# Kernel optimization log

Measured on AMD Instinct MI355X. Metric: run time of the kernel, lower is better.

## Reference

```python
import jax, jax.numpy as jnp
import numpy as np

B, C, H, W = 4, 256, 64, 64


def setup_inputs() -> dict:
    key = jax.random.key(0)
    ks = jax.random.split(key, 6)
    scale = 1.0 / np.sqrt(C)  # keep logits in a sane range
    x = jax.random.normal(ks[0], (B, C, H, W), dtype=jnp.float32)
    wq = jax.random.normal(ks[1], (C, C), dtype=jnp.float32) * scale
    wk = jax.random.normal(ks[2], (C, C), dtype=jnp.float32) * scale
    wv = jax.random.normal(ks[3], (C, C), dtype=jnp.float32) * scale
    wp = jax.random.normal(ks[4], (C, C), dtype=jnp.float32) * scale
    zb = jnp.zeros((C,), dtype=jnp.float32)
    return {"x": x, "wq": wq, "bq": zb, "wk": wk, "bk": zb,
            "wv": wv, "bv": zb, "wp": wp, "bp": zb}


def reference(x, wq, bq, wk, bk, wv, bv, wp, bp):
    b, c, h, w = x.shape
    n = h * w
    xf = x.reshape(b, c, n)  # [b, c, n] spatial tokens
    # 1x1 convs == channel-mixing GEMMs (weight layout: [out_c, in_c])
    q = jnp.einsum('oc,bcn->bon', wq, xf) + bq[:, None]
    k = jnp.einsum('oc,bcn->bon', wk, xf) + bk[:, None]
    v = jnp.einsum('oc,bcn->bon', wv, xf) + bv[:, None]
    # attn[b,i,j] = sum_c q[b,c,i] * k[b,c,j], scaled by c**-0.5
    logits = jnp.einsum('bci,bcj->bij', q, k) * (c ** -0.5)
    attn = jax.nn.softmax(logits, axis=-1)  # [b, n, n]
    # out[b,c,i] = sum_j attn[b,i,j] * v[b,c,j]
    out = jnp.einsum('bij,bcj->bci', attn, v)
    proj = jnp.einsum('oc,bcn->bon', wp, out) + bp[:, None]
    return x + proj.reshape(b, c, h, w)
```

## Files before the change

### kernel.cpp

```cpp
#include <hip/hip_runtime.h>
#include <hip/hip_bf16.h>


typedef __attribute__((ext_vector_type(4))) short s16x4;
typedef __attribute__((ext_vector_type(8))) short s16x8;
typedef __attribute__((ext_vector_type(16))) float f32x16;
typedef __attribute__((ext_vector_type(4))) int i32x4;
typedef __attribute__((ext_vector_type(8))) int i32x8;

#define MFMA32(a, b, c)   __builtin_amdgcn_mfma_f32_32x32x16_bf16((a), (b), (c), 0, 0, 0)
#define MFMASC(a, b, c) __builtin_amdgcn_mfma_scale_f32_32x32x64_f8f6f4((a), (b), (c), 0, 0, 0, 127, 0, 127)

constexpr int Cc = 256;
constexpr int Nn = 4096;

__device__ inline short f2bf(float f) {
    unsigned int u = __builtin_bit_cast(unsigned int, f);
    u = (u + 0x7fffu + ((u >> 16) & 1u)) >> 16;
    return (short)u;
}
__device__ inline unsigned char f2fp8(float f) {
    return (unsigned char)(__builtin_amdgcn_cvt_pk_fp8_f32(f, f, 0, false) & 0xff);
}
__device__ inline i32x8 cat8(i32x4 lo, i32x4 hi) {
    i32x8 r;
    r[0] = lo[0]; r[1] = lo[1]; r[2] = lo[2]; r[3] = lo[3];
    r[4] = hi[0]; r[5] = hi[1]; r[6] = hi[2]; r[7] = hi[3];
    return r;
}

__device__ inline void gl_lds16(const void* g, void* l) {
    __builtin_amdgcn_global_load_lds((const unsigned int*)g, (unsigned int*)l, 16, 0, 0);
}


#define WFRAG(Wm, row, kc) (*(const s16x8*)&(Wm)[(size_t)(kc)*2048 + (size_t)(row)*8])

__global__ __launch_bounds__(256, 4) void wcvt_kernel(
    const float* __restrict__ wq, const float* __restrict__ wk,
    const float* __restrict__ wv, const float* __restrict__ wp,
    short* __restrict__ W)
{
    const int m = blockIdx.y;
    const float* src = (m == 0) ? wq : (m == 1) ? wk : (m == 2) ? wv : wp;
    const int idx = (blockIdx.x * 256 + threadIdx.x) * 8;
    const int o = idx >> 8, c0 = idx & 255;
    float4 a = *(const float4*)(src + idx);
    float4 b = *(const float4*)(src + idx + 4);
    s16x8 p = { f2bf(a.x), f2bf(a.y), f2bf(a.z), f2bf(a.w),
                f2bf(b.x), f2bf(b.y), f2bf(b.z), f2bf(b.w) };
    *(s16x8*)(W + m * 65536 + ((size_t)(c0 >> 3) * 256 + o) * 8) = p;
}

__global__ __launch_bounds__(256, 4) void qkv_kernel(
    const float* __restrict__ x, const short* __restrict__ W,
    const float* __restrict__ bk, const float* __restrict__ bv,
    unsigned char* __restrict__ KT, unsigned char* __restrict__ V)
{
    const int nt = blockIdx.x, b = blockIdx.y, mat = blockIdx.z;
    const int n0 = nt * 64;
    const short* Wm = W + (mat + 1) * 65536;
    const float* bias = (mat == 0) ? bk : bv;
    const int t = threadIdx.x, lane = t & 63, wid = t >> 6, h = lane >> 5, l31 = lane & 31;

    __shared__ alignas(16) short xT[64][264];

    const float* xb = x + (size_t)b * Cc * Nn;
    #pragma unroll
    for (int r = 0; r < 16; ++r) {
        int g = r * 256 + t;
        int n = g & 63, cg = g >> 6;
        float f0 = xb[(size_t)(4*cg + 0) * Nn + n0 + n];
        float f1 = xb[(size_t)(4*cg + 1) * Nn + n0 + n];
        float f2 = xb[(size_t)(4*cg + 2) * Nn + n0 + n];
        float f3 = xb[(size_t)(4*cg + 3) * Nn + n0 + n];
        s16x4 p = { f2bf(f0), f2bf(f1), f2bf(f2), f2bf(f3) };
        *(s16x4*)&xT[n][4*cg] = p;
    }
    __syncthreads();

    f32x16 acc[4];
    #pragma unroll
    for (int s = 0; s < 4; ++s)
        #pragma unroll
        for (int r = 0; r < 16; ++r) acc[s][r] = 0.f;

    if (mat == 0) {
        const int mw = wid & 1, nwb = (wid >> 1) * 4;
        #pragma unroll 4
        for (int kk = 0; kk < 16; ++kk) {
            s16x8 a = *(const s16x8*)&xT[mw*32 + l31][kk*16 + h*8];
            #pragma unroll
            for (int s = 0; s < 4; ++s) {
                s16x8 bb = WFRAG(Wm, (nwb + s)*32 + l31, kk*2 + h);
                acc[s] = MFMA32(a, bb, acc[s]);
            }
        }
        unsigned char* dst = KT + (size_t)b * Nn * Cc;
        #pragma unroll
        for (int s = 0; s < 4; ++s) {
            int o = (nwb + s)*32 + l31;
            float bia = bias[o];
            #pragma unroll
            for (int r = 0; r < 16; ++r) {
                int n = mw*32 + (r & 3) + 8*(r >> 2) + 4*h;
                dst[(size_t)(n0 + n) * Cc + o] = f2fp8(acc[s][r] + bia);
            }
        }
    } else {
        #pragma unroll 4
        for (int kk = 0; kk < 16; ++kk) {
            s16x8 a0 = WFRAG(Wm, (wid*2 + 0)*32 + l31, kk*2 + h);
            s16x8 a1 = WFRAG(Wm, (wid*2 + 1)*32 + l31, kk*2 + h);
            s16x8 b0 = *(const s16x8*)&xT[ 0 + l31][kk*16 + h*8];
            s16x8 b1 = *(const s16x8*)&xT[32 + l31][kk*16 + h*8];
            acc[0] = MFMA32(a0, b0, acc[0]);
            acc[1] = MFMA32(a0, b1, acc[1]);
            acc[2] = MFMA32(a1, b0, acc[2]);
            acc[3] = MFMA32(a1, b1, acc[3]);
        }
        unsigned char* dst = V + (size_t)b * Cc * Nn;
        #pragma unroll
        for (int sub = 0; sub < 4; ++sub) {
            int mc = sub >> 1, nc = sub & 1;
            int j = n0 + nc*32 + l31;
            #pragma unroll
            for (int r = 0; r < 16; ++r) {
                int o = (wid*2 + mc)*32 + (r & 3) + 8*(r >> 2) + 4*h;
                dst[(((size_t)(j >> 3) * 256 + o) << 3) + (j & 7)] = f2fp8(acc[sub][r] + bias[o]);
            }
        }
    }
}

__global__ __launch_bounds__(512, 2) void attn_kernel(
    const unsigned char* __restrict__ KTg, const unsigned char* __restrict__ Vg,
    const short* __restrict__ Wg, const float* __restrict__ bq,
    const float* __restrict__ bp, const float* __restrict__ xg,
    float* __restrict__ outg)
{
    const int bid = blockIdx.x;
    const int b  = (bid & 7) >> 1;
    const int qt = ((bid >> 3) << 1) | (bid & 1);
    const int i0 = qt * 64;

    const int t = threadIdx.x, lane = t & 63, wid = t >> 6, h = lane >> 5, l31 = lane & 31;

    __shared__ alignas(16) char LDS[66304];
    char* KsB = LDS;
    unsigned char* FqB = (unsigned char*)(LDS + 32768);
    char* PsB = LDS + 49152;
    float* lpart = (float*)(LDS + 65536);
    float* linv  = (float*)(LDS + 66048);

    const unsigned char* Kb = KTg + (size_t)b * Nn * Cc;
    const unsigned char* Vb = Vg  + (size_t)b * Cc * Nn;
    const float* xb = xg + (size_t)b * Cc * Nn;

    const float SC = 0.09016844005f;
    f32x16 oacc[4];

    {
        short* xTp = (short*)LDS;
        #pragma unroll
        for (int r = 0; r < 8; ++r) {
            int g = r * 512 + t;
            int n = g & 63, cg = g >> 6;
            float f0 = xb[(size_t)(4*cg + 0) * Nn + i0 + n];
            float f1 = xb[(size_t)(4*cg + 1) * Nn + i0 + n];
            float f2 = xb[(size_t)(4*cg + 2) * Nn + i0 + n];
            float f3 = xb[(size_t)(4*cg + 3) * Nn + i0 + n];
            s16x4 p = { f2bf(f0), f2bf(f1), f2bf(f2), f2bf(f3) };
            int bcol = (((cg >> 1) ^ (n & 15)) << 4) + (cg & 1) * 8;
            *(s16x4*)((char*)xTp + n * 512 + bcol) = p;
        }
        __syncthreads();

        const short* Wq = Wg;
        f32x16 qa[2];
        #pragma unroll
        for (int s = 0; s < 2; ++s)
            #pragma unroll
            for (int r = 0; r < 16; ++r) qa[s][r] = 0.f;
        #pragma unroll 4
        for (int kk = 0; kk < 16; ++kk) {
            int gsw = ((kk*2 + h) ^ (l31 & 15)) << 4;
            s16x8 a0 = *(const s16x8*)((char*)xTp + ( 0 + l31) * 512 + gsw);
            s16x8 a1 = *(const s16x8*)((char*)xTp + (32 + l31) * 512 + gsw);
            s16x8 bb = WFRAG(Wq, wid*32 + l31, kk*2 + h);
            qa[0] = MFMA32(a0, bb, qa[0]);
            qa[1] = MFMA32(a1, bb, qa[1]);
        }
        const int o = wid*32 + l31;
        const float bo = bq[o];
        #pragma unroll
        for (int mw2 = 0; mw2 < 2; ++mw2)
            #pragma unroll
            for (int r = 0; r < 16; ++r) {
                int n = mw2*32 + (r & 3) + 8*(r >> 2) + 4*h;
                FqB[n*256 + (((o >> 4) ^ (n & 15)) << 4) + (o & 15)] = f2fp8(qa[mw2][r] + bo);
            }
    }
    __syncthreads();

    if (wid < 4) {
        const int w4 = wid, mj = w4 >> 1, ni = w4 & 1;

        i32x8 qf[4];
        {
            const int qrow = ni*32 + l31, qsw = qrow & 15;
            #pragma unroll
            for (int q = 0; q < 4; ++q) {
                i32x4 lo = *(const i32x4*)(FqB + qrow*256 + (((q*4 + h*2 + 0) ^ qsw) << 4));
                i32x4 hi = *(const i32x4*)(FqB + qrow*256 + (((q*4 + h*2 + 1) ^ qsw) << 4));
                qf[q] = cat8(lo, hi);
            }
        }
        float lacc = 0.f;
        const int rl = mj*32 + l31;
        const int ip = ni*32 + l31;
        const int rsw = rl & 15;

        for (int tt = 0; tt < 66; ++tt) {
            if (tt < 64) {
                const int kb = tt & 1;
                #pragma unroll
                for (int it = 0; it < 4; ++it) {
                    int r = w4*16 + it*4 + (lane >> 4);
                    int g = (lane & 15) ^ (r & 15);
                    const unsigned char* gp = Kb + (size_t)(tt*64 + r) * Cc + g*16;
                    char* lp = KsB + kb*16384 + (w4*16 + it*4)*256;
                    gl_lds16(gp, lp);
                }
            }
            if (tt >= 1 && tt < 65) {
                const int jt = tt - 1, kb = jt & 1;
                const char* abase = KsB + kb*16384 + rl*256;
                f32x16 s;
                #pragma unroll
                for (int r = 0; r < 16; ++r) s[r] = 0.f;
                #pragma unroll
                for (int q = 0; q < 4; ++q) {
                    i32x4 lo = *(const i32x4*)(abase + (((q*4 + h*2 + 0) ^ rsw) << 4));
                    i32x4 hi = *(const i32x4*)(abase + (((q*4 + h*2 + 1) ^ rsw) << 4));
                    s = MFMASC(cat8(lo, hi), qf[q], s);
                }
                float ps[16], lsum = 0.f;
                #pragma unroll
                for (int r = 0; r < 16; ++r) {
                    float e = exp2f(s[r] * SC);
                    ps[r] = e; lsum += e;
                }
                lsum += __shfl_xor(lsum, 32);
                lacc += lsum;
                char* pw = PsB + kb*5120 + ip*80 + mj*32 + 4*h;
                #pragma unroll
                for (int g = 0; g < 4; ++g) {
                    int w = __builtin_amdgcn_cvt_pk_fp8_f32(ps[4*g+0], ps[4*g+1], 0, false);
                    w = __builtin_amdgcn_cvt_pk_fp8_f32(ps[4*g+2], ps[4*g+3], w, true);
                    *(int*)(pw + g*8) = w;
                }
            }
            __syncthreads();
        }
        if (h == 0) lpart[mj*64 + ip] = lacc;
    } else {
        const int w2 = wid - 4;
        #pragma unroll
        for (int s = 0; s < 4; ++s)
            #pragma unroll
            for (int r = 0; r < 16; ++r) oacc[s][r] = 0.f;

        i32x8 vA0, vA1, vB0, vB1;
        const unsigned char* vb0 = Vb + (size_t)(w2*64 +  0 + l31) * 8;
        const unsigned char* vb1 = Vb + (size_t)(w2*64 + 32 + l31) * 8;

        for (int tp = 0; tp < 33; ++tp) {
            const int t0 = tp*2, t1 = t0 + 1;
            if (t0 >= 1 && t0 <= 64) {
                const size_t jc = (size_t)(t0 - 1) * 8;
                #pragma unroll
                for (int m = 0; m < 4; ++m) {
                    long v0 = *(const long*)(vb0 + (jc + h*4 + m) * 2048);
                    long v1 = *(const long*)(vb1 + (jc + h*4 + m) * 2048);
                    vA0[2*m] = (int)v0; vA0[2*m+1] = (int)((unsigned long)v0 >> 32);
                    vA1[2*m] = (int)v1; vA1[2*m+1] = (int)((unsigned long)v1 >> 32);
                }
            }
            if (t0 >= 2) {
                const int pb = (t0 - 2) & 1;
                const char* pr = PsB + pb*5120 + l31*80 + h*32;
                i32x8 p0 = cat8(*(const i32x4*)(pr),        *(const i32x4*)(pr + 16));
                i32x8 p1 = cat8(*(const i32x4*)(pr + 2560), *(const i32x4*)(pr + 2576));
                oacc[0] = MFMASC(vB0, p0, oacc[0]);
                oacc[1] = MFMASC(vB0, p1, oacc[1]);
                oacc[2] = MFMASC(vB1, p0, oacc[2]);
                oacc[3] = MFMASC(vB1, p1, oacc[3]);
            }
            asm volatile("s_barrier" ::: "memory");
            if (t1 <= 64) {
                const size_t jc = (size_t)(t1 - 1) * 8;
                #pragma unroll
                for (int m = 0; m < 4; ++m) {
                    long v0 = *(const long*)(vb0 + (jc + h*4 + m) * 2048);
                    long v1 = *(const long*)(vb1 + (jc + h*4 + m) * 2048);
                    vB0[2*m] = (int)v0; vB0[2*m+1] = (int)((unsigned long)v0 >> 32);
                    vB1[2*m] = (int)v1; vB1[2*m+1] = (int)((unsigned long)v1 >> 32);
                }
            }
            if (t1 >= 2) {
                const int pb = (t1 - 2) & 1;
                const char* pr = PsB + pb*5120 + l31*80 + h*32;
                i32x8 p0 = cat8(*(const i32x4*)(pr),        *(const i32x4*)(pr + 16));
                i32x8 p1 = cat8(*(const i32x4*)(pr + 2560), *(const i32x4*)(pr + 2576));
                oacc[0] = MFMASC(vA0, p0, oacc[0]);
                oacc[1] = MFMASC(vA0, p1, oacc[1]);
                oacc[2] = MFMASC(vA1, p0, oacc[2]);
                oacc[3] = MFMASC(vA1, p1, oacc[3]);
            }
            asm volatile("s_barrier" ::: "memory");
        }
    }

    __syncthreads();
    if (t < 64) linv[t] = 1.0f / (lpart[t] + lpart[64 + t]);
    __syncthreads();
    short (*T)[264] = (short(*)[264])LDS;
    if (wid >= 4) {
        const int w2 = wid - 4;
        #pragma unroll
        for (int sub = 0; sub < 4; ++sub) {
            int mc = sub >> 1, nc = sub & 1;
            int ip = nc*32 + l31;
            float rl2 = linv[ip];
            #pragma unroll
            for (int r = 0; r < 16; ++r) {
                int c = w2*64 + mc*32 + (r & 3) + 8*(r >> 2) + 4*h;
                T[ip][c] = f2bf(oacc[sub][r] * rl2);
            }
        }
    }
    __syncthreads();

    {
        const short* Wp = Wg + 3 * 65536;
        f32x16 acc2[2];
        #pragma unroll
        for (int s = 0; s < 2; ++s)
            #pragma unroll
            for (int r = 0; r < 16; ++r) acc2[s][r] = 0.f;

        #pragma unroll 4
        for (int kk = 0; kk < 16; ++kk) {
            s16x8 a0 = *(const s16x8*)&T[ 0 + l31][kk*16 + h*8];
            s16x8 a1 = *(const s16x8*)&T[32 + l31][kk*16 + h*8];
            s16x8 bb = WFRAG(Wp, wid*32 + l31, kk*2 + h);
            acc2[0] = MFMA32(a0, bb, acc2[0]);
            acc2[1] = MFMA32(a1, bb, acc2[1]);
        }
        __syncthreads();

        float (*F)[256] = (float(*)[256])LDS;
        {
            const int o = wid*32 + l31;
            #pragma unroll
            for (int nh = 0; nh < 2; ++nh) {
                #pragma unroll
                for (int r = 0; r < 16; ++r) {
                    int n = nh*32 + (r & 3) + 8*(r >> 2) + 4*h;
                    F[n][o ^ (n & 31)] = acc2[nh][r];
                }
            }
        }
        __syncthreads();

        float* ob = outg + (size_t)b * Cc * Nn;
        #pragma unroll 8
        for (int it = 0; it < 32; ++it) {
            int o = it*8 + wid;
            size_t idx = (size_t)o * Nn + i0 + lane;
            ob[idx] = xb[idx] + F[lane][o ^ (lane & 31)] + bp[o];
        }
    }
}

extern "C" void kernel_launch(void* const* d_in, const int* in_sizes, int n_in,
                              void* d_out, int out_size, void* d_ws, size_t ws_size,
                              hipStream_t stream)
{
    const float* x  = (const float*)d_in[0];
    const float* wq = (const float*)d_in[1];
    const float* bq = (const float*)d_in[2];
    const float* wk = (const float*)d_in[3];
    const float* bk = (const float*)d_in[4];
    const float* wv = (const float*)d_in[5];
    const float* bv = (const float*)d_in[6];
    const float* wp = (const float*)d_in[7];
    const float* bp = (const float*)d_in[8];

    const size_t kvbytes = (size_t)4 * Nn * Cc;
    const size_t wel     = (size_t)4 * 65536;
    const size_t need    = 2 * kvbytes + wel * sizeof(short);
    if (ws_size < need) return;
    unsigned char* KT = (unsigned char*)d_ws;
    unsigned char* V  = KT + kvbytes;
    short* Wbf = (short*)(V + kvbytes);
    (void)in_sizes; (void)n_in; (void)out_size;

    wcvt_kernel<<<dim3(32, 4), 256, 0, stream>>>(wq, wk, wv, wp, Wbf);
    qkv_kernel<<<dim3(64, 4, 2), 256, 0, stream>>>(x, Wbf, bk, bv, KT, V);
    attn_kernel<<<dim3(256), 512, 0, stream>>>(KT, V, Wbf, bq, bp, x, (float*)d_out);
}
```

Before: 168.3 us.

## Use FP8 MFMA for K/V projections and fold softmax scale into Q

The weight-conversion kernel now also writes FP8 copies of Wk and Wv. The K/V projection kernel stages x in LDS as FP8 with an XOR swizzle and uses the scaled 32x32x64 FP8 MFMA instead of bf16 MFMA, cutting instruction count and LDS/global bytes. In attention, Q is pre-multiplied by log2(e) before FP8 quantization and the 1/sqrt(C) factor moves into the MFMA scale exponent, which removes a multiply per logit. The per-tile row-sum shuffle is also hoisted out of the loop. The risk is reduced projection accuracy from FP8 inputs.

```diff
diff --git a/kernel.cpp b/kernel.cpp
--- a/kernel.cpp
+++ b/kernel.cpp
@@ -9,7 +9,8 @@
 typedef __attribute__((ext_vector_type(8))) int i32x8;
 
 #define MFMA32(a, b, c)   __builtin_amdgcn_mfma_f32_32x32x16_bf16((a), (b), (c), 0, 0, 0)
-#define MFMASC(a, b, c) __builtin_amdgcn_mfma_scale_f32_32x32x64_f8f6f4((a), (b), (c), 0, 0, 0, 127, 0, 127)
+#define MFMASC(a, b, c)   __builtin_amdgcn_mfma_scale_f32_32x32x64_f8f6f4((a), (b), (c), 0, 0, 0, 127, 0, 127)
+#define MFMASC_Q(a, b, c) __builtin_amdgcn_mfma_scale_f32_32x32x64_f8f6f4((a), (b), (c), 0, 0, 0, 123, 0, 127)
 
 constexpr int Cc = 256;
 constexpr int Nn = 4096;
@@ -35,11 +36,12 @@
 
 
 #define WFRAG(Wm, row, kc) (*(const s16x8*)&(Wm)[(size_t)(kc)*2048 + (size_t)(row)*8])
+#define WF8(Wf, row, g) (*(const i32x4*)&(Wf)[((size_t)(g)*256 + (row)) * 16])
 
 __global__ __launch_bounds__(256, 4) void wcvt_kernel(
     const float* __restrict__ wq, const float* __restrict__ wk,
     const float* __restrict__ wv, const float* __restrict__ wp,
-    short* __restrict__ W)
+    short* __restrict__ W, unsigned char* __restrict__ W8f)
 {
     const int m = blockIdx.y;
     const float* src = (m == 0) ? wq : (m == 1) ? wk : (m == 2) ? wv : wp;
@@ -50,20 +52,29 @@
     s16x8 p = { f2bf(a.x), f2bf(a.y), f2bf(a.z), f2bf(a.w),
                 f2bf(b.x), f2bf(b.y), f2bf(b.z), f2bf(b.w) };
     *(s16x8*)(W + m * 65536 + ((size_t)(c0 >> 3) * 256 + o) * 8) = p;
+    if (m == 1 || m == 2) {
+        unsigned char* Wf = W8f + (m - 1) * 65536;
+        int w0 = __builtin_amdgcn_cvt_pk_fp8_f32(a.x, a.y, 0, false);
+        w0 = __builtin_amdgcn_cvt_pk_fp8_f32(a.z, a.w, w0, true);
+        int w1 = __builtin_amdgcn_cvt_pk_fp8_f32(b.x, b.y, 0, false);
+        w1 = __builtin_amdgcn_cvt_pk_fp8_f32(b.z, b.w, w1, true);
+        unsigned char* dst = Wf + (((size_t)(c0 >> 4) * 256 + o) * 16) + (c0 & 15);
+        *(int*)(dst) = w0; *(int*)(dst + 4) = w1;
+    }
 }
 
 __global__ __launch_bounds__(256, 4) void qkv_kernel(
-    const float* __restrict__ x, const short* __restrict__ W,
+    const float* __restrict__ x, const unsigned char* __restrict__ W8f,
     const float* __restrict__ bk, const float* __restrict__ bv,
     unsigned char* __restrict__ KT, unsigned char* __restrict__ V)
 {
     const int nt = blockIdx.x, b = blockIdx.y, mat = blockIdx.z;
     const int n0 = nt * 64;
-    const short* Wm = W + (mat + 1) * 65536;
+    const unsigned char* Wf = W8f + mat * 65536;
     const float* bias = (mat == 0) ? bk : bv;
     const int t = threadIdx.x, lane = t & 63, wid = t >> 6, h = lane >> 5, l31 = lane & 31;
 
-    __shared__ alignas(16) short xT[64][264];
+    __shared__ alignas(16) unsigned char xT[64 * 256];
 
     const float* xb = x + (size_t)b * Cc * Nn;
     #pragma unroll
@@ -74,8 +85,9 @@
         float f1 = xb[(size_t)(4*cg + 1) * Nn + n0 + n];
         float f2 = xb[(size_t)(4*cg + 2) * Nn + n0 + n];
         float f3 = xb[(size_t)(4*cg + 3) * Nn + n0 + n];
-        s16x4 p = { f2bf(f0), f2bf(f1), f2bf(f2), f2bf(f3) };
-        *(s16x4*)&xT[n][4*cg] = p;
+        int w = __builtin_amdgcn_cvt_pk_fp8_f32(f0, f1, 0, false);
+        w = __builtin_amdgcn_cvt_pk_fp8_f32(f2, f3, w, true);
+        *(int*)(xT + n*256 + ((((cg >> 2) ^ (n & 15)) << 4) | (4*cg & 15))) = w;
     }
     __syncthreads();
 
@@ -87,13 +99,17 @@
 
     if (mat == 0) {
         const int mw = wid & 1, nwb = (wid >> 1) * 4;
-        #pragma unroll 4
-        for (int kk = 0; kk < 16; ++kk) {
-            s16x8 a = *(const s16x8*)&xT[mw*32 + l31][kk*16 + h*8];
+        const int arow = mw*32 + l31, asw = arow & 15;
+        #pragma unroll
+        for (int q = 0; q < 4; ++q) {
+            i32x4 alo = *(const i32x4*)(xT + arow*256 + (((q*4 + h*2 + 0) ^ asw) << 4));
+            i32x4 ahi = *(const i32x4*)(xT + arow*256 + (((q*4 + h*2 + 1) ^ asw) << 4));
+            i32x8 a = cat8(alo, ahi);
             #pragma unroll
             for (int s = 0; s < 4; ++s) {
-                s16x8 bb = WFRAG(Wm, (nwb + s)*32 + l31, kk*2 + h);
-                acc[s] = MFMA32(a, bb, acc[s]);
+                int o = (nwb + s)*32 + l31;
+                i32x8 bb = cat8(WF8(Wf, o, q*4 + h*2 + 0), WF8(Wf, o, q*4 + h*2 + 1));
+                acc[s] = MFMASC(a, bb, acc[s]);
             }
         }
         unsigned char* dst = KT + (size_t)b * Nn * Cc;
@@ -108,16 +124,20 @@
             }
         }
     } else {
-        #pragma unroll 4
-        for (int kk = 0; kk < 16; ++kk) {
-            s16x8 a0 = WFRAG(Wm, (wid*2 + 0)*32 + l31, kk*2 + h);
-            s16x8 a1 = WFRAG(Wm, (wid*2 + 1)*32 + l31, kk*2 + h);
-            s16x8 b0 = *(const s16x8*)&xT[ 0 + l31][kk*16 + h*8];
-            s16x8 b1 = *(const s16x8*)&xT[32 + l31][kk*16 + h*8];
-            acc[0] = MFMA32(a0, b0, acc[0]);
-            acc[1] = MFMA32(a0, b1, acc[1]);
-            acc[2] = MFMA32(a1, b0, acc[2]);
-            acc[3] = MFMA32(a1, b1, acc[3]);
+        const int b0r = 0 + l31, b1r = 32 + l31;
+        #pragma unroll
+        for (int q = 0; q < 4; ++q) {
+            int g0 = q*4 + h*2 + 0, g1 = q*4 + h*2 + 1;
+            i32x8 a0 = cat8(WF8(Wf, (wid*2 + 0)*32 + l31, g0), WF8(Wf, (wid*2 + 0)*32 + l31, g1));
+            i32x8 a1 = cat8(WF8(Wf, (wid*2 + 1)*32 + l31, g0), WF8(Wf, (wid*2 + 1)*32 + l31, g1));
+            i32x8 b0 = cat8(*(const i32x4*)(xT + b0r*256 + ((g0 ^ (b0r & 15)) << 4)),
+                            *(const i32x4*)(xT + b0r*256 + ((g1 ^ (b0r & 15)) << 4)));
+            i32x8 b1 = cat8(*(const i32x4*)(xT + b1r*256 + ((g0 ^ (b1r & 15)) << 4)),
+                            *(const i32x4*)(xT + b1r*256 + ((g1 ^ (b1r & 15)) << 4)));
+            acc[0] = MFMASC(a0, b0, acc[0]);
+            acc[1] = MFMASC(a0, b1, acc[1]);
+            acc[2] = MFMASC(a1, b0, acc[2]);
+            acc[3] = MFMASC(a1, b1, acc[3]);
         }
         unsigned char* dst = V + (size_t)b * Cc * Nn;
         #pragma unroll
@@ -157,7 +177,7 @@
     const unsigned char* Vb = Vg  + (size_t)b * Cc * Nn;
     const float* xb = xg + (size_t)b * Cc * Nn;
 
-    const float SC = 0.09016844005f;
+    const float L2E = 1.4426950408889634f;
     f32x16 oacc[4];
 
     {
@@ -198,7 +218,8 @@
             #pragma unroll
             for (int r = 0; r < 16; ++r) {
                 int n = mw2*32 + (r & 3) + 8*(r >> 2) + 4*h;
-                FqB[n*256 + (((o >> 4) ^ (n & 15)) << 4) + (o & 15)] = f2fp8(qa[mw2][r] + bo);
+                FqB[n*256 + (((o >> 4) ^ (n & 15)) << 4) + (o & 15)] =
+                    f2fp8((qa[mw2][r] + bo) * L2E);
             }
     }
     __syncthreads();
@@ -243,15 +264,14 @@
                 for (int q = 0; q < 4; ++q) {
                     i32x4 lo = *(const i32x4*)(abase + (((q*4 + h*2 + 0) ^ rsw) << 4));
                     i32x4 hi = *(const i32x4*)(abase + (((q*4 + h*2 + 1) ^ rsw) << 4));
-                    s = MFMASC(cat8(lo, hi), qf[q], s);
+                    s = MFMASC_Q(cat8(lo, hi), qf[q], s);
                 }
                 float ps[16], lsum = 0.f;
                 #pragma unroll
                 for (int r = 0; r < 16; ++r) {
-                    float e = exp2f(s[r] * SC);
+                    float e = exp2f(s[r]);
                     ps[r] = e; lsum += e;
                 }
-                lsum += __shfl_xor(lsum, 32);
                 lacc += lsum;
                 char* pw = PsB + kb*5120 + ip*80 + mj*32 + 4*h;
                 #pragma unroll
@@ -263,6 +283,7 @@
             }
             __syncthreads();
         }
+        lacc += __shfl_xor(lacc, 32);
         if (h == 0) lpart[mj*64 + ip] = lacc;
     } else {
         const int w2 = wid - 4;
@@ -400,14 +421,16 @@
 
     const size_t kvbytes = (size_t)4 * Nn * Cc;
     const size_t wel     = (size_t)4 * 65536;
-    const size_t need    = 2 * kvbytes + wel * sizeof(short);
+    const size_t wfb     = (size_t)2 * 65536;
+    const size_t need    = 2 * kvbytes + wel * sizeof(short) + wfb;
     if (ws_size < need) return;
     unsigned char* KT = (unsigned char*)d_ws;
     unsigned char* V  = KT + kvbytes;
     short* Wbf = (short*)(V + kvbytes);
+    unsigned char* W8f = (unsigned char*)(Wbf + wel);
     (void)in_sizes; (void)n_in; (void)out_size;
 
-    wcvt_kernel<<<dim3(32, 4), 256, 0, stream>>>(wq, wk, wv, wp, Wbf);
-    qkv_kernel<<<dim3(64, 4, 2), 256, 0, stream>>>(x, Wbf, bk, bv, KT, V);
+    wcvt_kernel<<<dim3(32, 4), 256, 0, stream>>>(wq, wk, wv, wp, Wbf, W8f);
+    qkv_kernel<<<dim3(64, 4, 2), 256, 0, stream>>>(x, W8f, bk, bv, KT, V);
     attn_kernel<<<dim3(256), 512, 0, stream>>>(KT, V, Wbf, bq, bp, x, (float*)d_out);
 }
```

Measured after the change: 152.4 us. 9.4% less time.
